# Optimization experiments

Hardware: AMD Instinct MI355X
Metric: run time of the kernel (lower is better)

Reference implementation:

```python
import jax, jax.numpy as jnp
import numpy as np

NUM_GRAPHS = 64
NEG_SLOPE_EDGE = 0.2   # GATLayer alpha
NEG_SLOPE_READ = 0.01  # torch default leaky_relu slope in ReadoutLayer


def leaky_relu(x, slope):
    return jnp.where(x >= 0, x, slope * x)


def segment_softmax(e, seg, n):
    # numerically stable softmax of edge logits grouped by destination node
    m = jax.ops.segment_max(e, seg, num_segments=n)
    m = jnp.where(jnp.isfinite(m), m, 0.0)  # guard nodes with no in-edges
    ex = jnp.exp(e - m[seg])
    s = jax.ops.segment_sum(ex, seg, num_segments=n)
    return ex / jnp.where(s > 0, s, 1.0)[seg]


def gat_layer(h, src, dst, e_feat, W, a):
    n = h.shape[0]
    out = W.shape[1]
    z = h @ W                                      # [N, out]
    a_src, a_dst, a_e = a[:out], a[out:2 * out], a[2 * out:]
    # concat([z_src, z_dst, e_feat]) @ a  ==  z_src@a_src + z_dst@a_dst + e@a_e
    logits = leaky_relu(z[src] @ a_src + z[dst] @ a_dst + e_feat @ a_e,
                        NEG_SLOPE_EDGE)            # [E]
    alpha = segment_softmax(logits, dst, n)        # [E]
    msg = alpha[:, None] * z[src]                  # [E, out]
    return jax.ops.segment_sum(msg, dst, num_segments=n)  # [N, out]


def readout(h, gid, w_att, b_att):
    # DGL mean_nodes(g, 'z', 'att'): multiply feat by weight, then mean per graph
    att = jnp.exp(leaky_relu(h @ w_att + b_att, NEG_SLOPE_READ))  # [N]
    num = jax.ops.segment_sum(att[:, None] * h, gid, num_segments=NUM_GRAPHS)
    cnt = jax.ops.segment_sum(jnp.ones_like(att), gid, num_segments=NUM_GRAPHS)
    return num / jnp.maximum(cnt, 1.0)[:, None]    # [G, hidden]


def setup_inputs() -> dict:
    key = jax.random.key(0)
    ks = jax.random.split(key, 16)
    N, E, F_IN, H, ED, C = 50000, 800000, 128, 128, 16, 10
    sc = lambda f: np.float32(1.0 / np.sqrt(f))
    return {
        "x": jax.random.normal(ks[0], (N, F_IN), jnp.float32),
        "e_feat": jax.random.normal(ks[1], (E, ED), jnp.float32),
        "src": jax.random.randint(ks[2], (E,), 0, N, dtype=jnp.int32),
        "dst": jax.random.randint(ks[3], (E,), 0, N, dtype=jnp.int32),
        "gid": jnp.sort(jax.random.randint(ks[4], (N,), 0, NUM_GRAPHS, dtype=jnp.int32)),
        "W1": jax.random.normal(ks[5], (F_IN, H), jnp.float32) * sc(F_IN),
        "a1": jax.random.normal(ks[6], (2 * H + ED,), jnp.float32) * sc(2 * H + ED),
        "W2": jax.random.normal(ks[7], (H, H), jnp.float32) * sc(H),
        "a2": jax.random.normal(ks[8], (2 * H + ED,), jnp.float32) * sc(2 * H + ED),
        "W3": jax.random.normal(ks[9], (H, H), jnp.float32) * sc(H),
        "a3": jax.random.normal(ks[10], (2 * H + ED,), jnp.float32) * sc(2 * H + ED),
        "w_att": jax.random.normal(ks[11], (H,), jnp.float32) * sc(H),
        "b_att": jnp.zeros((), jnp.float32),
        "W_cls": jax.random.normal(ks[12], (3 * H, C), jnp.float32) * sc(3 * H),
        "b_cls": jnp.zeros((C,), jnp.float32),
    }


def reference(x, e_feat, src, dst, gid, W1, a1, W2, a2, W3, a3,
              w_att, b_att, W_cls, b_cls):
    # dropout is identity at inference (training=False)
    h1 = jax.nn.relu(gat_layer(x, src, dst, e_feat, W1, a1))
    hg1 = readout(h1, gid, w_att, b_att)
    h2 = jax.nn.relu(gat_layer(h1, src, dst, e_feat, W2, a2))
    hg2 = readout(h2, gid, w_att, b_att)
    h3 = jax.nn.relu(gat_layer(h2, src, dst, e_feat, W3, a3))
    hg3 = readout(h3, gid, w_att, b_att)
    y = jnp.concatenate([hg1, hg2, hg3], axis=1) @ W_cls + b_cls  # [G, C]
    return jax.nn.log_softmax(y, axis=1)
```

## Files before the change

kernel.cpp:

```cpp
#include <hip/hip_runtime.h>
#include <math.h>

#define HD 128
#define ED 16
#define NG 64
#define NC 10
#define HK 8

typedef short bf16x8 __attribute__((ext_vector_type(8)));
typedef float f32x4 __attribute__((ext_vector_type(4)));

__device__ __forceinline__ unsigned short f2b(float x){
  unsigned u = __float_as_uint(x);
  unsigned r = (u + 0x7fffu + ((u >> 16) & 1u)) >> 16;
  return (unsigned short)r;
}
__device__ __forceinline__ float blo(unsigned p){ return __uint_as_float(p << 16); }
__device__ __forceinline__ float bhi(unsigned p){ return __uint_as_float(p & 0xffff0000u); }
__device__ __forceinline__ float bperm_f(int idx, float v){
  return __int_as_float(__builtin_amdgcn_ds_bpermute(idx<<2, __float_as_int(v)));
}
__device__ __forceinline__ int bperm_i(int idx, int v){
  return __builtin_amdgcn_ds_bpermute(idx<<2, v);
}

__global__ __launch_bounds__(256) void k_pre(
    const int* __restrict__ dst, int* __restrict__ h, int Nr,
    int* __restrict__ rank, int E, int NH,
    const float* __restrict__ x, unsigned short* __restrict__ xb,
    const float* __restrict__ W1, const float* __restrict__ W2, const float* __restrict__ W3,
    unsigned short* __restrict__ Wb,
    const int* __restrict__ gid, float* __restrict__ cnt,
    float* __restrict__ hg,
    int N, int ncast){
  int b = blockIdx.x;
  if(b < NH){
    int* hk = h + (size_t)(b & (HK-1))*Nr;
    int e4 = (b*256 + threadIdx.x)*4;
    if(e4+3 < E){
      int4 d = *(const int4*)&dst[e4];
      int4 r;
      r.x = atomicAdd(&hk[d.x], 1);
      r.y = atomicAdd(&hk[d.y], 1);
      r.z = atomicAdd(&hk[d.z], 1);
      r.w = atomicAdd(&hk[d.w], 1);
      *(int4*)&rank[e4] = r;
    } else {
      for(int k=0;k<4;k++) if(e4+k<E) rank[e4+k] = atomicAdd(&hk[dst[e4+k]], 1);
    }
    return;
  }
  b -= NH;
  if(b < ncast){
    int i = (b*256 + threadIdx.x)*8;
    if(i >= N*HD) return;
    float4 v0 = *(const float4*)&x[i];
    float4 v1 = *(const float4*)&x[i+4];
    uint4 o;
    o.x = f2b(v0.x) | ((unsigned)f2b(v0.y)<<16);
    o.y = f2b(v0.z) | ((unsigned)f2b(v0.w)<<16);
    o.z = f2b(v1.x) | ((unsigned)f2b(v1.y)<<16);
    o.w = f2b(v1.z) | ((unsigned)f2b(v1.w)<<16);
    *(uint4*)&xb[i] = o;
    return;
  }
  b -= ncast;
  if(b < 24){
    int idx = b*256 + threadIdx.x;
    if(idx >= 3*2048) return;
    int layer = idx >> 11;
    int r = idx & 2047;
    const float* W = (layer==0)?W1:((layer==1)?W2:W3);
    int lane = r & 63, tile = r >> 6;
    int kt = tile >> 3, nt = tile & 7;
    int qq = lane >> 4, cc = lane & 15;
    int kbase = kt*32 + qq*8;
    int col = nt*16 + cc;
    unsigned short tmp[8];
    #pragma unroll
    for(int j=0;j<8;j++) tmp[j] = f2b(W[(size_t)(kbase+j)*HD + col]);
    uint4 o;
    o.x = tmp[0]|((unsigned)tmp[1]<<16); o.y = tmp[2]|((unsigned)tmp[3]<<16);
    o.z = tmp[4]|((unsigned)tmp[5]<<16); o.w = tmp[6]|((unsigned)tmp[7]<<16);
    *(uint4*)&Wb[(size_t)idx*8] = o;
    return;
  }
  if(b == 24){
    int g = threadIdx.x;
    if(g >= NG) return;
    int lo=0, hi=N;
    while(lo<hi){ int mid=(lo+hi)>>1; if(gid[mid] < g) lo=mid+1; else hi=mid; }
    int start = lo; lo = start; hi = N;
    while(lo<hi){ int mid=(lo+hi)>>1; if(gid[mid] < g+1) lo=mid+1; else hi=mid; }
    cnt[g] = (float)(lo - start);
    return;
  }
  int i = ((b-25)*256 + threadIdx.x)*4;
  *(float4*)&hg[i] = (float4){0.f,0.f,0.f,0.f};
}

__global__ __launch_bounds__(64) void k_bsum(const int* __restrict__ h, int Nr,
                                             int* __restrict__ deg,
                                             int* __restrict__ bsum, int N){
  int b = blockIdx.x, t = threadIdx.x;
  int i = b*256 + t*4;
  int d0=0,d1=0,d2=0,d3=0;
  if(i+3 < N){
    #pragma unroll
    for(int k=0;k<HK;k++){
      int4 v = *(const int4*)&h[(size_t)k*Nr + i];
      d0+=v.x; d1+=v.y; d2+=v.z; d3+=v.w;
    }
    int4 o; o.x=d0; o.y=d1; o.z=d2; o.w=d3;
    *(int4*)&deg[i] = o;
  } else {
    int tmp[4] = {0,0,0,0};
    for(int j=0;j<4;j++) if(i+j<N){
      int s2=0;
      for(int k=0;k<HK;k++) s2 += h[(size_t)k*Nr + i + j];
      deg[i+j]=s2; tmp[j]=s2;
    }
    d0=tmp[0]; d1=tmp[1]; d2=tmp[2]; d3=tmp[3];
  }
  int s = d0+d1+d2+d3;
  #pragma unroll
  for(int o=32;o;o>>=1) s += __shfl_xor(s,o);
  if(t==0) bsum[b] = s;
}

__global__ __launch_bounds__(256) void k_bprop2(const int* __restrict__ deg,
                                                const int* __restrict__ bsum,
                                                const int* __restrict__ h, int Nr,
                                                int* __restrict__ offs,
                                                int* __restrict__ offs2,
                                                int N, int E){
  __shared__ int sh[256];
  __shared__ int sbase;
  int b = blockIdx.x, t = threadIdx.x;
  int s = 0;
  for(int j=t; j<b; j+=256) s += bsum[j];
  #pragma unroll
  for(int o=32;o;o>>=1) s += __shfl_xor(s,o);
  if(t < 4) sh[t] = 0;
  __syncthreads();
  if((t&63)==0) sh[t>>6] = s;
  __syncthreads();
  if(t==0) sbase = sh[0]+sh[1]+sh[2]+sh[3];
  __syncthreads();
  int i = b*256 + t;
  int v = (i<N) ? deg[i] : 0;
  sh[t] = v; __syncthreads();
  for(int o=1;o<256;o<<=1){ int u = (t>=o)?sh[t-o]:0; __syncthreads(); sh[t]+=u; __syncthreads(); }
  if(i<N){
    int base = sbase + sh[t] - v;
    offs[i] = base;
    int run = base;
    #pragma unroll
    for(int k=0;k<HK;k++){
      offs2[(size_t)i*HK + k] = run;
      run += h[(size_t)k*Nr + i];
    }
  }
  if(b==0 && t==0) offs[N] = E;
}


__device__ __forceinline__ void scatter_dev(int bidx,
                           const int* __restrict__ src, const int* __restrict__ dst,
                           const int* __restrict__ rank,
                           const float* __restrict__ ef,
                           const float* __restrict__ a1e, const float* __restrict__ a2e,
                           const float* __restrict__ a3e,
                           const int* __restrict__ offs2, uint2* __restrict__ rec, int E){
  int t = bidx*256 + threadIdx.x;
  int e = t >> 2;
  int sub = t & 3;
  if(e >= E) return;
  float4 f  = *(const float4*)&ef[(size_t)e*ED + sub*4];
  float4 A1 = *(const float4*)&a1e[sub*4];
  float4 A2 = *(const float4*)&a2e[sub*4];
  float4 A3 = *(const float4*)&a3e[sub*4];
  float q1 = fmaf(f.x,A1.x, fmaf(f.y,A1.y, fmaf(f.z,A1.z, f.w*A1.w)));
  float q2 = fmaf(f.x,A2.x, fmaf(f.y,A2.y, fmaf(f.z,A2.z, f.w*A2.w)));
  float q3 = fmaf(f.x,A3.x, fmaf(f.y,A3.y, fmaf(f.z,A3.z, f.w*A3.w)));
  q1 += __shfl_xor(q1,1); q1 += __shfl_xor(q1,2);
  q2 += __shfl_xor(q2,1); q2 += __shfl_xor(q2,2);
  q3 += __shfl_xor(q3,1); q3 += __shfl_xor(q3,2);
  if(sub == 0){
    int d = dst[e];
    int k = (e >> 10) & (HK-1);
    int p = offs2[((size_t)d<<3) | k] + rank[e];
    uint2 A;
    A.x = (unsigned)f2b(q1) | ((unsigned)f2b(q2) << 16);
    A.y = (unsigned)src[e] | ((unsigned)f2b(q3) << 16);
    rec[p] = A;
  }
}

__device__ __forceinline__ void gemm_dev(int bidx,
    const unsigned short* __restrict__ Ab,
    const unsigned short* __restrict__ Wb,
    unsigned short* __restrict__ Zb,
    const float* __restrict__ avec,
    float* __restrict__ ps, float* __restrict__ pd, int M)
{
  int tid = threadIdx.x;
  int w = tid >> 6, lane = tid & 63;
  int q = lane >> 4, c = lane & 15;
  int rowbase = bidx*128 + w*32;
  f32x4 acc[2][8];
  #pragma unroll
  for(int t=0;t<2;t++)
    #pragma unroll
    for(int n=0;n<8;n++) acc[t][n] = (f32x4){0.f,0.f,0.f,0.f};

  int r0 = rowbase + c;      if(r0 > M-1) r0 = M-1;
  int r1 = rowbase + 16 + c; if(r1 > M-1) r1 = M-1;
  #pragma unroll
  for(int kt=0; kt<4; kt++){
    int ko = kt*32 + q*8;
    bf16x8 a0 = __builtin_bit_cast(bf16x8, *(const uint4*)&Ab[(size_t)r0*HD + ko]);
    bf16x8 a1 = __builtin_bit_cast(bf16x8, *(const uint4*)&Ab[(size_t)r1*HD + ko]);
    #pragma unroll
    for(int n=0;n<8;n++){
      bf16x8 b = __builtin_bit_cast(bf16x8, *(const uint4*)&Wb[(((size_t)(kt*8+n))*64 + lane)*8]);
      acc[0][n] = __builtin_amdgcn_mfma_f32_16x16x32_bf16(a0, b, acc[0][n], 0,0,0);
      acc[1][n] = __builtin_amdgcn_mfma_f32_16x16x32_bf16(a1, b, acc[1][n], 0,0,0);
    }
  }
  float asv[8], adv[8];
  #pragma unroll
  for(int n=0;n<8;n++){ asv[n] = avec[n*16+c]; adv[n] = avec[HD + n*16+c]; }
  #pragma unroll
  for(int t=0;t<2;t++){
    #pragma unroll
    for(int r=0;r<4;r++){
      int grow = rowbase + t*16 + 4*q + r;
      bool ok = grow < M;
      #pragma unroll
      for(int n=0;n<8;n++){
        if(ok) Zb[(size_t)grow*HD + n*16 + c] = f2b(acc[t][n][r]);
      }
      float pp = 0.f, dd = 0.f;
      #pragma unroll
      for(int n=0;n<8;n++){ pp = fmaf(acc[t][n][r], asv[n], pp); dd = fmaf(acc[t][n][r], adv[n], dd); }
      #pragma unroll
      for(int o=1;o<16;o<<=1){ pp += __shfl_xor(pp,o); dd += __shfl_xor(dd,o); }
      if(ok && c==0){ ps[grow] = pp; pd[grow] = dd; }
    }
  }
}

#define RCH 16
__device__ __forceinline__ void readout_dev(int rb,
                          const unsigned* __restrict__ hbu,
                          const float* __restrict__ att,
                          const int* __restrict__ gid,
                          float* __restrict__ hg, int N){
  int g = rb >> 2;
  int chunk = ((rb & 3) << 2) + (threadIdx.x >> 6);
  int t = threadIdx.x & 63;
  int lo=0, hi=N;
  while(lo<hi){ int mid=(lo+hi)>>1; if(gid[mid] < g) lo=mid+1; else hi=mid; }
  int start = lo; lo = start; hi = N;
  while(lo<hi){ int mid=(lo+hi)>>1; if(gid[mid] < g+1) lo=mid+1; else hi=mid; }
  int end = lo;
  int len = end - start;
  int c0 = start + (int)(((long long)len * chunk) / RCH);
  int c1 = start + (int)(((long long)len * (chunk+1)) / RCH);
  float acc0 = 0.f, acc1 = 0.f;
  for(int v=c0; v<c1; v++){
    unsigned P = hbu[(size_t)v*64 + t];
    float a = att[v];
    acc0 = fmaf(a, blo(P), acc0);
    acc1 = fmaf(a, bhi(P), acc1);
  }
  atomicAdd(&hg[g*HD + 2*t],     acc0);
  atomicAdd(&hg[g*HD + 2*t + 1], acc1);
}

__global__ __launch_bounds__(256) void k_sg1(
    const unsigned short* __restrict__ Ab, const unsigned short* __restrict__ Wb,
    unsigned short* __restrict__ Zb, const float* __restrict__ avec,
    float* __restrict__ ps, float* __restrict__ pd, int M, int GB,
    const int* __restrict__ src, const int* __restrict__ dst, const int* __restrict__ rank,
    const float* __restrict__ ef, const float* __restrict__ a1e, const float* __restrict__ a2e,
    const float* __restrict__ a3e, const int* __restrict__ offs2, uint2* __restrict__ rec, int E){
  if(blockIdx.x < GB) gemm_dev(blockIdx.x, Ab, Wb, Zb, avec, ps, pd, M);
  else scatter_dev(blockIdx.x - GB, src, dst, rank, ef, a1e, a2e, a3e, offs2, rec, E);
}

__global__ __launch_bounds__(256) void k_rg(
    const unsigned short* __restrict__ Ab, const unsigned short* __restrict__ Wb,
    unsigned short* __restrict__ Zb, const float* __restrict__ avec,
    float* __restrict__ ps, float* __restrict__ pd, int M, int GB,
    const unsigned* __restrict__ hbu, const float* __restrict__ att,
    const int* __restrict__ gid, float* __restrict__ hg, int N){
  if(blockIdx.x < GB) gemm_dev(blockIdx.x, Ab, Wb, Zb, avec, ps, pd, M);
  else readout_dev(blockIdx.x - GB, hbu, att, gid, hg, N);
}

__global__ __launch_bounds__(256) void k_agg2(const uint4* __restrict__ zb4,
                                              const int* __restrict__ offs,
                                              const uint2* __restrict__ rec,
                                              const float* __restrict__ ps,
                                              const float* __restrict__ pd,
                                              int layer,
                                              unsigned* __restrict__ hbu,
                                              float* __restrict__ att,
                                              const float* __restrict__ watt,
                                              const float* __restrict__ batt, int N){
  int wid = blockIdx.x*4 + (threadIdx.x>>6);
  int lane = threadIdx.x & 63;
  if(wid >= N) return;
  int q = lane >> 4, c = lane & 15;
  int d0 = offs[wid], d1 = offs[wid+1];
  float pdv = pd[wid];
  float acc[8];
  #pragma unroll
  for(int i=0;i<8;i++) acc[i]=0.f;
  float ssum = 0.f;

  for(int t0=d0; t0<d1; t0+=64){
    int rem = d1 - t0; if(rem > 64) rem = 64;
    int j = t0 + lane;
    float w = 0.f; int u = 0;
    if(j < d1){
      uint2 R = rec[j];
      u = (int)(R.y & 0xffffu);
      unsigned qb = (layer==0) ? (R.x & 0xffffu) : (layer==1 ? (R.x >> 16) : (R.y >> 16));
      float ql = __uint_as_float(qb << 16);
      float l = ps[u] + pdv + ql;
      l = (l >= 0.f) ? l : 0.2f*l;
      w = __expf(l);
    }
    float ws = w;
    #pragma unroll
    for(int o=32;o;o>>=1) ws += __shfl_xor(ws,o);
    ssum += ws;
    for(int jb=0; jb<rem; jb+=16){
      float w0 = bperm_f(jb+q,    w);  int u0 = bperm_i(jb+q,    u);
      float w1 = bperm_f(jb+4+q,  w);  int u1 = bperm_i(jb+4+q,  u);
      float w2 = bperm_f(jb+8+q,  w);  int u2 = bperm_i(jb+8+q,  u);
      float w3 = bperm_f(jb+12+q, w);  int u3 = bperm_i(jb+12+q, u);
      uint4 P0 = zb4[(size_t)u0*16 + c];
      uint4 P1 = zb4[(size_t)u1*16 + c];
      uint4 P2 = zb4[(size_t)u2*16 + c];
      uint4 P3 = zb4[(size_t)u3*16 + c];
      acc[0] = fmaf(w0, blo(P0.x), acc[0]); acc[1] = fmaf(w0, bhi(P0.x), acc[1]);
      acc[2] = fmaf(w0, blo(P0.y), acc[2]); acc[3] = fmaf(w0, bhi(P0.y), acc[3]);
      acc[4] = fmaf(w0, blo(P0.z), acc[4]); acc[5] = fmaf(w0, bhi(P0.z), acc[5]);
      acc[6] = fmaf(w0, blo(P0.w), acc[6]); acc[7] = fmaf(w0, bhi(P0.w), acc[7]);
      acc[0] = fmaf(w1, blo(P1.x), acc[0]); acc[1] = fmaf(w1, bhi(P1.x), acc[1]);
      acc[2] = fmaf(w1, blo(P1.y), acc[2]); acc[3] = fmaf(w1, bhi(P1.y), acc[3]);
      acc[4] = fmaf(w1, blo(P1.z), acc[4]); acc[5] = fmaf(w1, bhi(P1.z), acc[5]);
      acc[6] = fmaf(w1, blo(P1.w), acc[6]); acc[7] = fmaf(w1, bhi(P1.w), acc[7]);
      acc[0] = fmaf(w2, blo(P2.x), acc[0]); acc[1] = fmaf(w2, bhi(P2.x), acc[1]);
      acc[2] = fmaf(w2, blo(P2.y), acc[2]); acc[3] = fmaf(w2, bhi(P2.y), acc[3]);
      acc[4] = fmaf(w2, blo(P2.z), acc[4]); acc[5] = fmaf(w2, bhi(P2.z), acc[5]);
      acc[6] = fmaf(w2, blo(P2.w), acc[6]); acc[7] = fmaf(w2, bhi(P2.w), acc[7]);
      acc[0] = fmaf(w3, blo(P3.x), acc[0]); acc[1] = fmaf(w3, bhi(P3.x), acc[1]);
      acc[2] = fmaf(w3, blo(P3.y), acc[2]); acc[3] = fmaf(w3, bhi(P3.y), acc[3]);
      acc[4] = fmaf(w3, blo(P3.z), acc[4]); acc[5] = fmaf(w3, bhi(P3.z), acc[5]);
      acc[6] = fmaf(w3, blo(P3.w), acc[6]); acc[7] = fmaf(w3, bhi(P3.w), acc[7]);
    }
  }
  #pragma unroll
  for(int i=0;i<8;i++){ acc[i] += __shfl_xor(acc[i],16); acc[i] += __shfl_xor(acc[i],32); }
  float inv = (d1 > d0) ? 1.0f/ssum : 0.0f;
  #pragma unroll
  for(int i=0;i<8;i++) acc[i] = fmaxf(acc[i]*inv, 0.f);
  hbu[(size_t)wid*64 + c*4 + q] = (unsigned)f2b(acc[2*q]) | ((unsigned)f2b(acc[2*q+1])<<16);
  float4 w0v = *(const float4*)&watt[c*8];
  float4 w1v = *(const float4*)&watt[c*8+4];
  float t = acc[0]*w0v.x + acc[1]*w0v.y + acc[2]*w0v.z + acc[3]*w0v.w
          + acc[4]*w1v.x + acc[5]*w1v.y + acc[6]*w1v.z + acc[7]*w1v.w;
  #pragma unroll
  for(int o=1;o<16;o<<=1) t += __shfl_xor(t,o);
  t += batt[0];
  float lr = (t >= 0.f) ? t : 0.01f*t;
  if(lane==0) att[wid] = __expf(lr);
}

__global__ __launch_bounds__(64) void k_readout(const unsigned* __restrict__ hbu,
                                                const float* __restrict__ att,
                                                const int* __restrict__ gid,
                                                float* __restrict__ hg, int N){
  int g = blockIdx.x / RCH;
  int chunk = blockIdx.x % RCH;
  int t = threadIdx.x;
  int lo=0, hi=N;
  while(lo<hi){ int mid=(lo+hi)>>1; if(gid[mid] < g) lo=mid+1; else hi=mid; }
  int start = lo; lo = start; hi = N;
  while(lo<hi){ int mid=(lo+hi)>>1; if(gid[mid] < g+1) lo=mid+1; else hi=mid; }
  int end = lo;
  int len = end - start;
  int c0 = start + (int)(((long long)len * chunk) / RCH);
  int c1 = start + (int)(((long long)len * (chunk+1)) / RCH);
  float acc0 = 0.f, acc1 = 0.f;
  for(int v=c0; v<c1; v++){
    unsigned P = hbu[(size_t)v*64 + t];
    float a = att[v];
    acc0 = fmaf(a, blo(P), acc0);
    acc1 = fmaf(a, bhi(P), acc1);
  }
  atomicAdd(&hg[g*HD + 2*t],     acc0);
  atomicAdd(&hg[g*HD + 2*t + 1], acc1);
}

__global__ __launch_bounds__(384) void k_final(const float* __restrict__ hg,
                                               const float* __restrict__ cnt,
                                               const float* __restrict__ Wc,
                                               const float* __restrict__ bc,
                                               float* __restrict__ out){
  int g = blockIdx.x;
  int t = threadIdx.x;
  __shared__ float red[6];
  __shared__ float yv[NC];
  float invc = 1.f / fmaxf(cnt[g], 1.f);
  int part = t >> 7;
  int f = t & 127;
  float v = hg[(size_t)part*NG*HD + g*HD + f] * invc;
  for(int c=0; c<NC; c++){
    float p = v * Wc[(size_t)t*NC + c];
    #pragma unroll
    for(int o=32;o;o>>=1) p += __shfl_xor(p,o);
    if((t&63)==0) red[t>>6] = p;
    __syncthreads();
    if(t==0) yv[c] = bc[c] + red[0]+red[1]+red[2]+red[3]+red[4]+red[5];
    __syncthreads();
  }
  if(t==0){
    float mx = -INFINITY;
    #pragma unroll
    for(int c=0;c<NC;c++) mx = fmaxf(mx, yv[c]);
    float s = 0.f;
    #pragma unroll
    for(int c=0;c<NC;c++) s += __expf(yv[c] - mx);
    float ls = logf(s);
    #pragma unroll
    for(int c=0;c<NC;c++) out[g*NC + c] = yv[c] - mx - ls;
  }
}

extern "C" void kernel_launch(void* const* d_in, const int* in_sizes, int n_in,
                              void* d_out, int out_size, void* d_ws, size_t ws_size,
                              hipStream_t stream) {
  const float* x     = (const float*)d_in[0];
  const float* efeat = (const float*)d_in[1];
  const int*   src   = (const int*)d_in[2];
  const int*   dst   = (const int*)d_in[3];
  const int*   gid   = (const int*)d_in[4];
  const float* W1    = (const float*)d_in[5];
  const float* a1    = (const float*)d_in[6];
  const float* W2    = (const float*)d_in[7];
  const float* a2    = (const float*)d_in[8];
  const float* W3    = (const float*)d_in[9];
  const float* a3    = (const float*)d_in[10];
  const float* watt  = (const float*)d_in[11];
  const float* batt  = (const float*)d_in[12];
  const float* Wc    = (const float*)d_in[13];
  const float* bc    = (const float*)d_in[14];
  float* out = (float*)d_out;

  int N = in_sizes[4];
  int E = in_sizes[2];
  int Nr = (N + 63) & ~63;

  char* p = (char*)d_ws;
  auto alloc = [&](size_t bytes)->void*{
    void* r = (void*)p;
    p += (bytes + 255) & ~(size_t)255;
    return r;
  };
  unsigned short* Xb = (unsigned short*)alloc((size_t)N*HD*2);
  unsigned short* Hb = (unsigned short*)alloc((size_t)N*HD*2);
  unsigned short* Zb = (unsigned short*)alloc((size_t)N*HD*2);
  unsigned short* Wball = (unsigned short*)alloc((size_t)3*2048*8*2);
  float* ps      = (float*)alloc((size_t)N*4);
  float* pd      = (float*)alloc((size_t)N*4);
  float* att     = (float*)alloc((size_t)N*4);
  int*   deg     = (int*)  alloc((size_t)N*4);
  int*   offs    = (int*)  alloc((size_t)(N+1)*4);
  int*   offs2   = (int*)  alloc((size_t)N*HK*4);
  int*   h       = (int*)  alloc((size_t)Nr*HK*4);
  int*   rank    = (int*)  alloc((size_t)E*4);
  uint2* rec     = (uint2*)alloc((size_t)E*8);
  int*   bsum    = (int*)  alloc((size_t)1024*4);
  float* hg      = (float*)alloc((size_t)3*NG*HD*4);
  float* cnt     = (float*)alloc((size_t)NG*4);
  (void)ws_size; (void)n_in; (void)out_size;

  int nwblocks = (N + 3) / 4;
  int nb = (N + 255) / 256;
  int ncast = (N*16 + 255) / 256;
  int NH = (E/4 + 255) / 256;
  int GB = (N + 127) / 128;
  int SB = (E*4 + 255) / 256;

  hipMemsetAsync(h, 0, (size_t)Nr*HK*4, stream);
  k_pre<<<NH + ncast + 49, 256, 0, stream>>>(dst, h, Nr, rank, E, NH,
                                             x, Xb, W1, W2, W3, Wball,
                                             gid, cnt, hg, N, ncast);
  k_bsum<<<nb, 64, 0, stream>>>(h, Nr, deg, bsum, N);
  k_bprop2<<<nb, 256, 0, stream>>>(deg, bsum, h, Nr, offs, offs2, N, E);
  k_sg1<<<GB + SB, 256, 0, stream>>>(Xb, Wball, Zb, a1, ps, pd, N, GB,
                                     src, dst, rank, efeat,
                                     a1+2*HD, a2+2*HD, a3+2*HD, offs2, rec, E);
  k_agg2<<<nwblocks, 256, 0, stream>>>((const uint4*)Zb, offs, rec, ps, pd, 0,
                                       (unsigned*)Hb, att, watt, batt, N);
  k_rg<<<GB + NG*4, 256, 0, stream>>>(Hb, Wball + (size_t)1*2048*8, Zb, a2, ps, pd, N, GB,
                                      (const unsigned*)Hb, att, gid, hg + 0*NG*HD, N);
  k_agg2<<<nwblocks, 256, 0, stream>>>((const uint4*)Zb, offs, rec, ps, pd, 1,
                                       (unsigned*)Hb, att, watt, batt, N);
  k_rg<<<GB + NG*4, 256, 0, stream>>>(Hb, Wball + (size_t)2*2048*8, Zb, a3, ps, pd, N, GB,
                                      (const unsigned*)Hb, att, gid, hg + 1*NG*HD, N);
  k_agg2<<<nwblocks, 256, 0, stream>>>((const uint4*)Zb, offs, rec, ps, pd, 2,
                                       (unsigned*)Hb, att, watt, batt, N);
  k_readout<<<NG*RCH, 64, 0, stream>>>((const unsigned*)Hb, att, gid,
                                       hg + 2*NG*HD, N);
  k_final<<<NG, 384, 0, stream>>>(hg, cnt, Wc, bc, out);
}
```

Baseline: 421.5 us.

## Shard degree histogram per XCC and precompute edge payloads in pre-pass

The degree-count atomics now pick their histogram copy by hardware XCC id and use workgroup-scope relaxed atomics, with the copy id packed into the rank's top byte. Edge-feature logit projections and src packing move into the pre-pass, writing a dense payload array. The scatter kernel then runs one thread per edge and only moves the payload to its CSR slot. offs2 becomes k-major. The aim is cheaper atomics with better cache locality and a lighter scatter kernel overlapped with the GEMM. The cost is an extra E*8-byte buffer round trip. Workgroup-scope atomics on memory shared across workgroups within one XCC rely on that XCC's L2 coherence, which is hardware-dependent.

```diff
diff --git a/kernel.cpp b/kernel.cpp
--- a/kernel.cpp
+++ b/kernel.cpp
@@ -26,7 +26,10 @@
 
 __global__ __launch_bounds__(256) void k_pre(
     const int* __restrict__ dst, int* __restrict__ h, int Nr,
-    int* __restrict__ rank, int E, int NH,
+    int* __restrict__ rank, int E, int NH, int NE4,
+    const int* __restrict__ src, const float* __restrict__ ef,
+    const float* __restrict__ a1e, const float* __restrict__ a2e,
+    const float* __restrict__ a3e, uint2* __restrict__ pay,
     const float* __restrict__ x, unsigned short* __restrict__ xb,
     const float* __restrict__ W1, const float* __restrict__ W2, const float* __restrict__ W3,
     unsigned short* __restrict__ Wb,
@@ -35,22 +38,51 @@
     int N, int ncast){
   int b = blockIdx.x;
   if(b < NH){
-    int* hk = h + (size_t)(b & (HK-1))*Nr;
+    int xcc;
+    asm volatile("s_getreg_b32 %0, hwreg(HW_REG_XCC_ID, 0, 4)" : "=s"(xcc));
+    xcc &= (HK-1);
+    int* hk = h + (size_t)xcc*Nr;
+    int tag = xcc << 24;
     int e4 = (b*256 + threadIdx.x)*4;
     if(e4+3 < E){
       int4 d = *(const int4*)&dst[e4];
       int4 r;
-      r.x = atomicAdd(&hk[d.x], 1);
-      r.y = atomicAdd(&hk[d.y], 1);
-      r.z = atomicAdd(&hk[d.z], 1);
-      r.w = atomicAdd(&hk[d.w], 1);
+      r.x = __hip_atomic_fetch_add(&hk[d.x], 1, __ATOMIC_RELAXED, __HIP_MEMORY_SCOPE_WORKGROUP) | tag;
+      r.y = __hip_atomic_fetch_add(&hk[d.y], 1, __ATOMIC_RELAXED, __HIP_MEMORY_SCOPE_WORKGROUP) | tag;
+      r.z = __hip_atomic_fetch_add(&hk[d.z], 1, __ATOMIC_RELAXED, __HIP_MEMORY_SCOPE_WORKGROUP) | tag;
+      r.w = __hip_atomic_fetch_add(&hk[d.w], 1, __ATOMIC_RELAXED, __HIP_MEMORY_SCOPE_WORKGROUP) | tag;
       *(int4*)&rank[e4] = r;
     } else {
-      for(int k=0;k<4;k++) if(e4+k<E) rank[e4+k] = atomicAdd(&hk[dst[e4+k]], 1);
+      for(int k=0;k<4;k++) if(e4+k<E)
+        rank[e4+k] = __hip_atomic_fetch_add(&hk[dst[e4+k]], 1, __ATOMIC_RELAXED, __HIP_MEMORY_SCOPE_WORKGROUP) | tag;
     }
     return;
   }
   b -= NH;
+  if(b < NE4){
+    int t = b*256 + threadIdx.x;
+    int e = t >> 2;
+    int sub = t & 3;
+    if(e >= E) return;
+    float4 f  = *(const float4*)&ef[(size_t)e*ED + sub*4];
+    float4 A1 = *(const float4*)&a1e[sub*4];
+    float4 A2 = *(const float4*)&a2e[sub*4];
+    float4 A3 = *(const float4*)&a3e[sub*4];
+    float q1 = fmaf(f.x,A1.x, fmaf(f.y,A1.y, fmaf(f.z,A1.z, f.w*A1.w)));
+    float q2 = fmaf(f.x,A2.x, fmaf(f.y,A2.y, fmaf(f.z,A2.z, f.w*A2.w)));
+    float q3 = fmaf(f.x,A3.x, fmaf(f.y,A3.y, fmaf(f.z,A3.z, f.w*A3.w)));
+    q1 += __shfl_xor(q1,1); q1 += __shfl_xor(q1,2);
+    q2 += __shfl_xor(q2,1); q2 += __shfl_xor(q2,2);
+    q3 += __shfl_xor(q3,1); q3 += __shfl_xor(q3,2);
+    if(sub == 0){
+      uint2 A;
+      A.x = (unsigned)f2b(q1) | ((unsigned)f2b(q2) << 16);
+      A.y = (unsigned)src[e] | ((unsigned)f2b(q3) << 16);
+      pay[e] = A;
+    }
+    return;
+  }
+  b -= NE4;
   if(b < ncast){
     int i = (b*256 + threadIdx.x)*8;
     if(i >= N*HD) return;
@@ -157,7 +189,7 @@
     int run = base;
     #pragma unroll
     for(int k=0;k<HK;k++){
-      offs2[(size_t)i*HK + k] = run;
+      offs2[(size_t)k*Nr + i] = run;
       run += h[(size_t)k*Nr + i];
     }
   }
@@ -166,35 +198,17 @@
 
 
 __device__ __forceinline__ void scatter_dev(int bidx,
-                           const int* __restrict__ src, const int* __restrict__ dst,
-                           const int* __restrict__ rank,
-                           const float* __restrict__ ef,
-                           const float* __restrict__ a1e, const float* __restrict__ a2e,
-                           const float* __restrict__ a3e,
-                           const int* __restrict__ offs2, uint2* __restrict__ rec, int E){
-  int t = bidx*256 + threadIdx.x;
-  int e = t >> 2;
-  int sub = t & 3;
+                           const int* __restrict__ dst, const int* __restrict__ rank,
+                           const uint2* __restrict__ pay,
+                           const int* __restrict__ offs2, int Nr,
+                           uint2* __restrict__ rec, int E){
+  int e = bidx*256 + threadIdx.x;
   if(e >= E) return;
-  float4 f  = *(const float4*)&ef[(size_t)e*ED + sub*4];
-  float4 A1 = *(const float4*)&a1e[sub*4];
-  float4 A2 = *(const float4*)&a2e[sub*4];
-  float4 A3 = *(const float4*)&a3e[sub*4];
-  float q1 = fmaf(f.x,A1.x, fmaf(f.y,A1.y, fmaf(f.z,A1.z, f.w*A1.w)));
-  float q2 = fmaf(f.x,A2.x, fmaf(f.y,A2.y, fmaf(f.z,A2.z, f.w*A2.w)));
-  float q3 = fmaf(f.x,A3.x, fmaf(f.y,A3.y, fmaf(f.z,A3.z, f.w*A3.w)));
-  q1 += __shfl_xor(q1,1); q1 += __shfl_xor(q1,2);
-  q2 += __shfl_xor(q2,1); q2 += __shfl_xor(q2,2);
-  q3 += __shfl_xor(q3,1); q3 += __shfl_xor(q3,2);
-  if(sub == 0){
-    int d = dst[e];
-    int k = (e >> 10) & (HK-1);
-    int p = offs2[((size_t)d<<3) | k] + rank[e];
-    uint2 A;
-    A.x = (unsigned)f2b(q1) | ((unsigned)f2b(q2) << 16);
-    A.y = (unsigned)src[e] | ((unsigned)f2b(q3) << 16);
-    rec[p] = A;
-  }
+  int d = dst[e];
+  unsigned rk = (unsigned)rank[e];
+  int k = (int)(rk >> 24);
+  int p = offs2[(size_t)k*Nr + d] + (int)(rk & 0xffffffu);
+  rec[p] = pay[e];
 }
 
 __device__ __forceinline__ void gemm_dev(int bidx,
@@ -283,11 +297,11 @@
     const unsigned short* __restrict__ Ab, const unsigned short* __restrict__ Wb,
     unsigned short* __restrict__ Zb, const float* __restrict__ avec,
     float* __restrict__ ps, float* __restrict__ pd, int M, int GB,
-    const int* __restrict__ src, const int* __restrict__ dst, const int* __restrict__ rank,
-    const float* __restrict__ ef, const float* __restrict__ a1e, const float* __restrict__ a2e,
-    const float* __restrict__ a3e, const int* __restrict__ offs2, uint2* __restrict__ rec, int E){
+    const int* __restrict__ dst, const int* __restrict__ rank,
+    const uint2* __restrict__ pay,
+    const int* __restrict__ offs2, int Nr, uint2* __restrict__ rec, int E){
   if(blockIdx.x < GB) gemm_dev(blockIdx.x, Ab, Wb, Zb, avec, ps, pd, M);
-  else scatter_dev(blockIdx.x - GB, src, dst, rank, ef, a1e, a2e, a3e, offs2, rec, E);
+  else scatter_dev(blockIdx.x - GB, dst, rank, pay, offs2, Nr, rec, E);
 }
 
 __global__ __launch_bounds__(256) void k_rg(
@@ -482,9 +496,10 @@
   float* att     = (float*)alloc((size_t)N*4);
   int*   deg     = (int*)  alloc((size_t)N*4);
   int*   offs    = (int*)  alloc((size_t)(N+1)*4);
-  int*   offs2   = (int*)  alloc((size_t)N*HK*4);
+  int*   offs2   = (int*)  alloc((size_t)Nr*HK*4);
   int*   h       = (int*)  alloc((size_t)Nr*HK*4);
   int*   rank    = (int*)  alloc((size_t)E*4);
+  uint2* pay     = (uint2*)alloc((size_t)E*8);
   uint2* rec     = (uint2*)alloc((size_t)E*8);
   int*   bsum    = (int*)  alloc((size_t)1024*4);
   float* hg      = (float*)alloc((size_t)3*NG*HD*4);
@@ -495,18 +510,19 @@
   int nb = (N + 255) / 256;
   int ncast = (N*16 + 255) / 256;
   int NH = (E/4 + 255) / 256;
+  int NE4 = (E*4 + 255) / 256;
   int GB = (N + 127) / 128;
-  int SB = (E*4 + 255) / 256;
+  int SB = (E + 255) / 256;
 
   hipMemsetAsync(h, 0, (size_t)Nr*HK*4, stream);
-  k_pre<<<NH + ncast + 49, 256, 0, stream>>>(dst, h, Nr, rank, E, NH,
-                                             x, Xb, W1, W2, W3, Wball,
-                                             gid, cnt, hg, N, ncast);
+  k_pre<<<NH + NE4 + ncast + 49, 256, 0, stream>>>(dst, h, Nr, rank, E, NH, NE4,
+                                                   src, efeat, a1+2*HD, a2+2*HD, a3+2*HD, pay,
+                                                   x, Xb, W1, W2, W3, Wball,
+                                                   gid, cnt, hg, N, ncast);
   k_bsum<<<nb, 64, 0, stream>>>(h, Nr, deg, bsum, N);
   k_bprop2<<<nb, 256, 0, stream>>>(deg, bsum, h, Nr, offs, offs2, N, E);
   k_sg1<<<GB + SB, 256, 0, stream>>>(Xb, Wball, Zb, a1, ps, pd, N, GB,
-                                     src, dst, rank, efeat,
-                                     a1+2*HD, a2+2*HD, a3+2*HD, offs2, rec, E);
+                                     dst, rank, pay, offs2, Nr, rec, E);
   k_agg2<<<nwblocks, 256, 0, stream>>>((const uint4*)Zb, offs, rec, ps, pd, 0,
                                        (unsigned*)Hb, att, watt, batt, N);
   k_rg<<<GB + NG*4, 256, 0, stream>>>(Hb, Wball + (size_t)1*2048*8, Zb, a2, ps, pd, N, GB,
```

After: 401.3 us. 1.05x faster.
